# Kernel optimization log

Measured on AMD Instinct MI355X. Metric: run time of the kernel, lower is better.

The kernel has to match this reference:

```python
import jax, jax.numpy as jnp
import numpy as np

N, E, D, H, C = 50000, 800000, 128, 128, 40
EPS = 1e-5


def setup_inputs() -> dict:
    key = jax.random.key(0)
    ks = jax.random.split(key, 18)
    s = lambda d: 1.0 / np.sqrt(d)
    inp = {
        "x": jax.random.normal(ks[0], (N, D), dtype=jnp.float32),
        "edge_index": jax.random.randint(ks[1], (2, E), 0, N, dtype=jnp.int64),
        # GCNConv weights (x @ W + b after normalized aggregation)
        "W1": jax.random.normal(ks[2], (D, H), dtype=jnp.float32) * s(D),
        "b1": jax.random.normal(ks[3], (H,), dtype=jnp.float32) * 0.01,
        "W2": jax.random.normal(ks[4], (H, H), dtype=jnp.float32) * s(H),
        "b2": jax.random.normal(ks[5], (H,), dtype=jnp.float32) * 0.01,
        "W3": jax.random.normal(ks[6], (H, H), dtype=jnp.float32) * s(H),
        "b3": jax.random.normal(ks[7], (H,), dtype=jnp.float32) * 0.01,
        # LayerNorm params (applied after layers 0 and 1 only)
        "ln1_g": 1.0 + 0.1 * jax.random.normal(ks[8], (H,), dtype=jnp.float32),
        "ln1_b": 0.1 * jax.random.normal(ks[9], (H,), dtype=jnp.float32),
        "ln2_g": 1.0 + 0.1 * jax.random.normal(ks[10], (H,), dtype=jnp.float32),
        "ln2_b": 0.1 * jax.random.normal(ks[11], (H,), dtype=jnp.float32),
        # post_mp MLP head
        "mpW1": jax.random.normal(ks[12], (H, H), dtype=jnp.float32) * s(H),
        "mpb1": jax.random.normal(ks[13], (H,), dtype=jnp.float32) * 0.01,
        "mpW2": jax.random.normal(ks[14], (H, C), dtype=jnp.float32) * s(H),
        "mpb2": jax.random.normal(ks[15], (C,), dtype=jnp.float32) * 0.01,
    }
    return inp


def _layernorm(h, g, b):
    mu = jnp.mean(h, axis=-1, keepdims=True)
    var = jnp.mean((h - mu) ** 2, axis=-1, keepdims=True)
    return (h - mu) * jax.lax.rsqrt(var + EPS) * g + b


def _gcn_forward(x, edge_index, params):
    (W1, b1, W2, b2, W3, b3, ln1_g, ln1_b, ln2_g, ln2_b, mpW1, mpb1, mpW2, mpb2) = params
    n = x.shape[0]
    loop = jnp.arange(n, dtype=edge_index.dtype)
    src = jnp.concatenate([edge_index[0], loop])  # source-to-target flow + self-loops
    dst = jnp.concatenate([edge_index[1], loop])
    deg = jax.ops.segment_sum(jnp.ones_like(src, dtype=x.dtype), dst, num_segments=n)
    dis = jax.lax.rsqrt(deg)  # deg >= 1 due to self-loops
    norm = dis[src] * dis[dst]  # [E+N]

    def conv(h, W, b):
        h = h @ W
        msg = h[src] * norm[:, None]  # gather + scale
        return jax.ops.segment_sum(msg, dst, num_segments=n) + b  # scatter-add

    h = x
    # layer 0
    h = conv(h, W1, b1)
    h = jax.nn.relu(h)  # dropout p=0.1 -> identity in eval
    h = _layernorm(h, ln1_g, ln1_b)
    # layer 1
    h = conv(h, W2, b2)
    h = jax.nn.relu(h)
    h = _layernorm(h, ln2_g, ln2_b)
    # layer 2 (emb is pre-relu conv output)
    emb = conv(h, W3, b3)
    h = jax.nn.relu(emb)
    # post_mp: Linear -> Dropout(eval: identity) -> Linear
    h = h @ mpW1 + mpb1
    logits = h @ mpW2 + mpb2
    return emb, jax.nn.log_softmax(logits, axis=1)


def reference(x, edge_index, W1, b1, W2, b2, W3, b3, ln1_g, ln1_b, ln2_g, ln2_b, mpW1, mpb1, mpW2, mpb2):
    params = (W1, b1, W2, b2, W3, b3, ln1_g, ln1_b, ln2_g, ln2_b, mpW1, mpb1, mpW2, mpb2)
    return _gcn_forward(x, edge_index, params)
```

## Files before the change

### kernel.cpp

```cpp
#include <hip/hip_runtime.h>

typedef __bf16 bf16x8 __attribute__((ext_vector_type(8)));
typedef float  f32x4  __attribute__((ext_vector_type(4)));
typedef unsigned short u16;
typedef unsigned int   u32;
typedef long long      i64;

#define BSH  7
#define BCAP 4096
#define NPB  256

__device__ __forceinline__ float b2f(u16 x){ return __uint_as_float(((u32)x) << 16); }
__device__ __forceinline__ u16 f2b(float x){
  u32 u = __float_as_uint(x);
  return (u16)((u + 0x7FFFu + ((u >> 16) & 1u)) >> 16);
}

__global__ __launch_bounds__(256) void k_detect(const u16* __restrict__ x,
                                                const u32* __restrict__ ei,
                                                int* __restrict__ flags){
  __shared__ int sh[2];
  int t = threadIdx.x;
  if (t < 2) sh[t] = 0;
  __syncthreads();
  int sane = 0;
  for (int i = t; i < 4096; i += 256){
    u16 u = x[i]; u32 e = (u >> 7) & 0xFFu;
    if (u == 0 || (e >= 0x70u && e <= 0x8Fu)) sane++;
  }
  int nz = 0;
  for (int i = t; i < 1024; i += 256)
    if (ei[2*i + 1] != 0u) nz++;
  atomicAdd(&sh[0], sane);
  atomicAdd(&sh[1], nz);
  __syncthreads();
  if (t == 0){
    flags[0] = (sh[0] < 3500) ? 1 : 0;
    flags[1] = (sh[1] == 0) ? 1 : 0;
  }
}

__device__ __forceinline__ int ld_idx(const void* ei, long long j, int is64){
  return is64 ? (int)((const i64*)ei)[j] : ((const int*)ei)[j];
}
__device__ __forceinline__ float ld_f(const void* p, int j, int isf32){
  return isf32 ? ((const float*)p)[j] : b2f(((const u16*)p)[j]);
}

__global__ __launch_bounds__(256) void k_partA(const void* __restrict__ ei, int E, int n,
                                               int* __restrict__ cntmat,
                                               const int* __restrict__ flags, int nbuk){
  __shared__ int cnt[512];
  int t = threadIdx.x;
  int is64 = flags[1];
  for (int i = t; i < 512; i += 256) cnt[i] = 0;
  __syncthreads();
  long long R = ((long long)E + NPB - 1) / NPB;
  long long lo = (long long)blockIdx.x * R;
  long long hi = lo + R; if (hi > E) hi = E;
  for (long long e = lo + t; e < hi; e += 256){
    int d = ld_idx(ei, (long long)E + e, is64);
    if ((unsigned)d < (unsigned)n) atomicAdd(&cnt[(unsigned)d >> BSH], 1);
  }
  __syncthreads();
  for (int b = t; b < nbuk; b += 256)
    cntmat[(size_t)b*NPB + blockIdx.x] = cnt[b];
}

__global__ __launch_bounds__(NPB) void k_scanBK(const int* __restrict__ cntmat,
                                                int* __restrict__ basemat,
                                                int* __restrict__ bcnt){
  __shared__ int sh[NPB];
  int b = blockIdx.x, t = threadIdx.x;
  int v = cntmat[(size_t)b*NPB + t];
  sh[t] = v; __syncthreads();
  for (int off = 1; off < NPB; off <<= 1){
    int u = 0; if (t >= off) u = sh[t - off];
    __syncthreads(); sh[t] += u; __syncthreads();
  }
  basemat[(size_t)b*NPB + t] = sh[t] - v;
  if (t == NPB-1) bcnt[b] = sh[t];
}

__global__ __launch_bounds__(256) void k_partC(const void* __restrict__ ei, int E, int n,
                                               const int* __restrict__ basemat,
                                               u32* __restrict__ ebuf,
                                               const int* __restrict__ flags, int nbuk){
  __shared__ int cur[512];
  int t = threadIdx.x;
  int is64 = flags[1];
  for (int i = t; i < 512; i += 256) cur[i] = 0;
  __syncthreads();
  for (int b = t; b < nbuk; b += 256) cur[b] = basemat[(size_t)b*NPB + blockIdx.x];
  __syncthreads();
  long long R = ((long long)E + NPB - 1) / NPB;
  long long lo = (long long)blockIdx.x * R;
  long long hi = lo + R; if (hi > E) hi = E;
  for (long long e = lo + t; e < hi; e += 256){
    int d = ld_idx(ei, (long long)E + e, is64);
    int s = ld_idx(ei, e, is64);
    if ((unsigned)d < (unsigned)n && (unsigned)s < (unsigned)n){
      int b = (unsigned)d >> BSH;
      int p = atomicAdd(&cur[b], 1);
      if (p < BCAP) ebuf[(size_t)b*BCAP + p] = (u32)s | ((u32)(d & ((1<<BSH)-1)) << 17);
    }
  }
}

__global__ __launch_bounds__(256) void k_bdeg(const int* __restrict__ bcnt,
                                              const u32* __restrict__ ebuf,
                                              int* __restrict__ deg, int n){
  __shared__ int cnt[1<<BSH];
  int b = blockIdx.x, t = threadIdx.x;
  if (t < (1<<BSH)) cnt[t] = 0;
  __syncthreads();
  int m = bcnt[b]; if (m > BCAP) m = BCAP;
  const u32* eb = ebuf + (size_t)b*BCAP;
  for (int i = t; i < m; i += 256)
    atomicAdd(&cnt[eb[i] >> 17], 1);
  __syncthreads();
  if (t < (1<<BSH)){
    int node = (b << BSH) + t;
    if (node < n) deg[node] = cnt[t];
  }
}

__global__ __launch_bounds__(256) void k_scanA(const int* __restrict__ deg, int n,
                                               int* __restrict__ bsum){
  __shared__ int sh[256];
  int t = threadIdx.x;
  int base = blockIdx.x*1024 + t*4;
  int s = 0;
  #pragma unroll
  for (int i = 0; i < 4; ++i){ int idx = base + i; if (idx < n) s += deg[idx]; }
  sh[t] = s; __syncthreads();
  for (int off = 128; off; off >>= 1){
    if (t < off) sh[t] += sh[t + off];
    __syncthreads();
  }
  if (t == 0) bsum[blockIdx.x] = sh[0];
}

__global__ __launch_bounds__(256) void k_scanB(int* __restrict__ bsum, int nB,
                                               int* __restrict__ rowptr, int n){
  __shared__ int sh[256];
  int t = threadIdx.x;
  int v = (t < nB) ? bsum[t] : 0;
  sh[t] = v; __syncthreads();
  for (int off = 1; off < 256; off <<= 1){
    int u = 0; if (t >= off) u = sh[t - off];
    __syncthreads(); sh[t] += u; __syncthreads();
  }
  if (t < nB) bsum[t] = sh[t] - v;
  if (t == 255) rowptr[n] = sh[255];
}

__global__ __launch_bounds__(256) void k_scanC(const int* __restrict__ deg, int n,
                                               const int* __restrict__ bsum,
                                               int* __restrict__ rowptr,
                                               float* __restrict__ dis){
  __shared__ int sh[256];
  int t = threadIdx.x;
  int base = blockIdx.x*1024 + t*4;
  int d[4]; int s = 0;
  #pragma unroll
  for (int i = 0; i < 4; ++i){ int idx = base + i; d[i] = (idx < n) ? deg[idx] : 0; s += d[i]; }
  sh[t] = s; __syncthreads();
  for (int off = 1; off < 256; off <<= 1){
    int u = 0; if (t >= off) u = sh[t - off];
    __syncthreads(); sh[t] += u; __syncthreads();
  }
  int run = bsum[blockIdx.x] + sh[t] - s;
  #pragma unroll
  for (int i = 0; i < 4; ++i){
    int idx = base + i;
    if (idx < n){
      rowptr[idx] = run; run += d[i];
      dis[idx] = rsqrtf((float)(d[i] + 1));
    }
  }
}

__global__ __launch_bounds__(256) void k_bfill(const int* __restrict__ bcnt,
                                               const u32* __restrict__ ebuf,
                                               const int* __restrict__ rowptr,
                                               int* __restrict__ colx, int n){
  __shared__ int cur[1<<BSH];
  int b = blockIdx.x, t = threadIdx.x;
  if (t < (1<<BSH)){
    int node = (b << BSH) + t;
    cur[t] = (node < n) ? rowptr[node] : 0;
  }
  __syncthreads();
  int m = bcnt[b]; if (m > BCAP) m = BCAP;
  const u32* eb = ebuf + (size_t)b*BCAP;
  for (int i = t; i < m; i += 256){
    u32 e = eb[i];
    int p = atomicAdd(&cur[e >> 17], 1);
    colx[p] = (int)(e & 0x1FFFFu);
  }
}

__global__ __launch_bounds__(64) void k_shufW(const void* __restrict__ W, u16* __restrict__ Ws,
                                              const int* __restrict__ flags){
  int f = flags[0];
  int bid = blockIdx.x;
  int nt = bid >> 2, kk = bid & 3;
  int l = threadIdx.x;
  int g = l >> 4, mr = l & 15;
  int nn = nt*16 + mr;
  #pragma unroll
  for (int i = 0; i < 8; ++i){
    int k = kk*32 + g*4 + (i & 3) + ((i >> 2) << 4);
    u16 w = f ? f2b(((const float*)W)[k*128 + nn]) : ((const u16*)W)[k*128 + nn];
    Ws[(size_t)(bid*64 + l)*8 + i] = w;
  }
}

__global__ __launch_bounds__(256) void k_gemm(const void* __restrict__ A, int aExt,
    const u16* __restrict__ Ws, const float* __restrict__ dis,
    u16* __restrict__ T, int nTiles, const int* __restrict__ flags)
{
  int wave = threadIdx.x >> 6, lane = threadIdx.x & 63;
  int tile = blockIdx.x*4 + wave;
  if (tile >= nTiles) return;
  int g = lane >> 4, mr = lane & 15;
  int f = aExt ? flags[0] : 0;
  union U8 { ushort4 q[2]; u16 s[8]; bf16x8 b; };
  bf16x8 a[4];
  if (f){
    const float* ap = (const float*)A + (size_t)(tile*16 + mr)*128;
    #pragma unroll
    for (int kk = 0; kk < 4; ++kk){
      float4 p = *(const float4*)(ap + kk*32 + g*4);
      float4 q = *(const float4*)(ap + kk*32 + g*4 + 16);
      U8 u;
      u.s[0]=f2b(p.x); u.s[1]=f2b(p.y); u.s[2]=f2b(p.z); u.s[3]=f2b(p.w);
      u.s[4]=f2b(q.x); u.s[5]=f2b(q.y); u.s[6]=f2b(q.z); u.s[7]=f2b(q.w);
      a[kk] = u.b;
    }
  } else {
    const u16* ap = (const u16*)A + (size_t)(tile*16 + mr)*128;
    #pragma unroll
    for (int kk = 0; kk < 4; ++kk){
      U8 u;
      u.q[0] = *(const ushort4*)(ap + kk*32 + g*4);
      u.q[1] = *(const ushort4*)(ap + kk*32 + g*4 + 16);
      a[kk] = u.b;
    }
  }
  float dj[4];
  #pragma unroll
  for (int j = 0; j < 4; ++j) dj[j] = dis[tile*16 + g*4 + j];
  #pragma unroll
  for (int nt = 0; nt < 8; ++nt){
    f32x4 acc = {0.f,0.f,0.f,0.f};
    #pragma unroll
    for (int kk = 0; kk < 4; ++kk){
      bf16x8 b = *(const bf16x8*)(Ws + (size_t)((nt*4 + kk)*64 + lane)*8);
      acc = __builtin_amdgcn_mfma_f32_16x16x32_bf16(a[kk], b, acc, 0, 0, 0);
    }
    int nn = nt*16 + mr;
    #pragma unroll
    for (int j = 0; j < 4; ++j){
      int row = tile*16 + g*4 + j;
      T[(size_t)row*128 + nn] = f2b(acc[j] * dj[j]);
    }
  }
}

template<int MODE>
__global__ __launch_bounds__(256) void k_agg(const u16* __restrict__ T,
    const int* __restrict__ rowptr, const int* __restrict__ colx,
    const float* __restrict__ dis, const void* __restrict__ bias,
    const void* __restrict__ lg, const void* __restrict__ lb,
    void* __restrict__ outA, int n, const int* __restrict__ flags)
{
  int wave = threadIdx.x >> 6, l = threadIdx.x & 63;
  int v = blockIdx.x*4 + wave; if (v >= n) return;
  int f = flags[0];
  int d0 = l*2;
  u32 self = *(const u32*)(T + (size_t)v*128 + d0);
  float p0 = b2f((u16)(self & 0xffff)), p1 = b2f((u16)(self >> 16));
  float q0 = 0.f, q1 = 0.f, r0 = 0.f, r1 = 0.f, t0 = 0.f, t1 = 0.f;
  int s = rowptr[v], e = rowptr[v+1];
  for (int base = s; base < e; base += 64){
    int cnt = e - base; if (cnt > 64) cnt = 64;
    int my = (base + l < e) ? colx[base + l] : 0;
    int i = 0;
    for (; i + 8 <= cnt; i += 8){
      int nb0 = __shfl(my, i),   nb1 = __shfl(my, i+1);
      int nb2 = __shfl(my, i+2), nb3 = __shfl(my, i+3);
      int nb4 = __shfl(my, i+4), nb5 = __shfl(my, i+5);
      int nb6 = __shfl(my, i+6), nb7 = __shfl(my, i+7);
      u32 u0 = *(const u32*)(T + (size_t)nb0*128 + d0);
      u32 u1 = *(const u32*)(T + (size_t)nb1*128 + d0);
      u32 u2 = *(const u32*)(T + (size_t)nb2*128 + d0);
      u32 u3 = *(const u32*)(T + (size_t)nb3*128 + d0);
      u32 u4 = *(const u32*)(T + (size_t)nb4*128 + d0);
      u32 u5 = *(const u32*)(T + (size_t)nb5*128 + d0);
      u32 u6 = *(const u32*)(T + (size_t)nb6*128 + d0);
      u32 u7 = *(const u32*)(T + (size_t)nb7*128 + d0);
      p0 += b2f((u16)(u0 & 0xffff)) + b2f((u16)(u4 & 0xffff));
      p1 += b2f((u16)(u0 >> 16))    + b2f((u16)(u4 >> 16));
      q0 += b2f((u16)(u1 & 0xffff)) + b2f((u16)(u5 & 0xffff));
      q1 += b2f((u16)(u1 >> 16))    + b2f((u16)(u5 >> 16));
      r0 += b2f((u16)(u2 & 0xffff)) + b2f((u16)(u6 & 0xffff));
      r1 += b2f((u16)(u2 >> 16))    + b2f((u16)(u6 >> 16));
      t0 += b2f((u16)(u3 & 0xffff)) + b2f((u16)(u7 & 0xffff));
      t1 += b2f((u16)(u3 >> 16))    + b2f((u16)(u7 >> 16));
    }
    for (; i + 4 <= cnt; i += 4){
      int nb0 = __shfl(my, i), nb1 = __shfl(my, i+1);
      int nb2 = __shfl(my, i+2), nb3 = __shfl(my, i+3);
      u32 u0 = *(const u32*)(T + (size_t)nb0*128 + d0);
      u32 u1 = *(const u32*)(T + (size_t)nb1*128 + d0);
      u32 u2 = *(const u32*)(T + (size_t)nb2*128 + d0);
      u32 u3 = *(const u32*)(T + (size_t)nb3*128 + d0);
      p0 += b2f((u16)(u0 & 0xffff)); p1 += b2f((u16)(u0 >> 16));
      q0 += b2f((u16)(u1 & 0xffff)); q1 += b2f((u16)(u1 >> 16));
      r0 += b2f((u16)(u2 & 0xffff)); r1 += b2f((u16)(u2 >> 16));
      t0 += b2f((u16)(u3 & 0xffff)); t1 += b2f((u16)(u3 >> 16));
    }
    for (; i < cnt; ++i){
      int nb = __shfl(my, i);
      u32 u = *(const u32*)(T + (size_t)nb*128 + d0);
      p0 += b2f((u16)(u & 0xffff)); p1 += b2f((u16)(u >> 16));
    }
  }
  float a0 = (p0 + q0) + (r0 + t0);
  float a1 = (p1 + q1) + (r1 + t1);
  float sc = dis[v];
  float x0 = fmaf(a0, sc, ld_f(bias, d0,   f));
  float x1 = fmaf(a1, sc, ld_f(bias, d0+1, f));
  if (MODE == 0){
    x0 = fmaxf(x0, 0.f); x1 = fmaxf(x1, 0.f);
    float sum = x0 + x1;
    #pragma unroll
    for (int off = 32; off; off >>= 1) sum += __shfl_xor(sum, off);
    float mu = sum * (1.f/128.f);
    float e0 = x0 - mu, e1 = x1 - mu;
    float vs = e0*e0 + e1*e1;
    #pragma unroll
    for (int off = 32; off; off >>= 1) vs += __shfl_xor(vs, off);
    float inv = rsqrtf(vs*(1.f/128.f) + 1e-5f);
    u16* oa = (u16*)outA;
    oa[(size_t)v*128 + d0]   = f2b(e0*inv*ld_f(lg, d0,   f) + ld_f(lb, d0,   f));
    oa[(size_t)v*128 + d0+1] = f2b(e1*inv*ld_f(lg, d0+1, f) + ld_f(lb, d0+1, f));
  } else {
    if (f){
      float* oa = (float*)outA;
      oa[(size_t)v*128 + d0]   = x0;
      oa[(size_t)v*128 + d0+1] = x1;
    } else {
      u16* oa = (u16*)outA;
      oa[(size_t)v*128 + d0]   = f2b(x0);
      oa[(size_t)v*128 + d0+1] = f2b(x1);
    }
  }
}

__global__ __launch_bounds__(128) void k_wc(const void* __restrict__ mpW1, const void* __restrict__ mpb1,
    const void* __restrict__ mpW2, const void* __restrict__ mpb2,
    float* __restrict__ Wc, float* __restrict__ bc, const int* __restrict__ flags)
{
  int f = flags[0];
  int c = blockIdx.x;
  int k = threadIdx.x;
  float acc = 0.f;
  if (f){
    const float* A  = (const float*)mpW1 + (size_t)k*128;
    const float* B2 = (const float*)mpW2;
    #pragma unroll 8
    for (int j = 0; j < 128; ++j) acc = fmaf(A[j], B2[j*40 + c], acc);
    if (k == 0){
      const float* b1p = (const float*)mpb1;
      float b = ((const float*)mpb2)[c];
      #pragma unroll 8
      for (int j = 0; j < 128; ++j) b = fmaf(b1p[j], B2[j*40 + c], b);
      bc[c] = b;
    }
  } else {
    const u16* A  = (const u16*)mpW1 + (size_t)k*128;
    const u16* B2 = (const u16*)mpW2;
    #pragma unroll 8
    for (int j = 0; j < 128; ++j) acc = fmaf(b2f(A[j]), b2f(B2[j*40 + c]), acc);
    if (k == 0){
      const u16* b1p = (const u16*)mpb1;
      float b = b2f(((const u16*)mpb2)[c]);
      #pragma unroll 8
      for (int j = 0; j < 128; ++j) b = fmaf(b2f(b1p[j]), b2f(B2[j*40 + c]), b);
      bc[c] = b;
    }
  }
  Wc[k*40 + c] = acc;
}

__global__ __launch_bounds__(64) void k_shufWc(const float* __restrict__ Wc, u16* __restrict__ Wcs){
  int bid = blockIdx.x;
  int nt = bid >> 2, kk = bid & 3;
  int l = threadIdx.x;
  int g = l >> 4, mr = l & 15;
  int nn = nt*16 + mr;
  #pragma unroll
  for (int i = 0; i < 8; ++i){
    int k = kk*32 + g*4 + (i & 3) + ((i >> 2) << 4);
    Wcs[(size_t)(bid*64 + l)*8 + i] = (nn < 40) ? f2b(Wc[k*40 + nn]) : (u16)0;
  }
}

__global__ __launch_bounds__(256) void k_logitsM(const u16* __restrict__ Wcs,
    const float* __restrict__ bc, void* __restrict__ dout, int n,
    const int* __restrict__ flags)
{
  int wave = threadIdx.x >> 6, lane = threadIdx.x & 63;
  int tile = blockIdx.x*4 + wave;
  int nTiles = n >> 4;
  if (tile >= nTiles) return;
  int f = flags[0];
  int g = lane >> 4, mr = lane & 15;
  union U8 { ushort4 q[2]; u16 s[8]; bf16x8 b; };
  bf16x8 a[4];
  if (f){
    const float* ap = (const float*)dout + (size_t)(tile*16 + mr)*128;
    #pragma unroll
    for (int kk = 0; kk < 4; ++kk){
      float4 p = *(const float4*)(ap + kk*32 + g*4);
      float4 q = *(const float4*)(ap + kk*32 + g*4 + 16);
      U8 u;
      u.s[0]=f2b(fmaxf(p.x,0.f)); u.s[1]=f2b(fmaxf(p.y,0.f));
      u.s[2]=f2b(fmaxf(p.z,0.f)); u.s[3]=f2b(fmaxf(p.w,0.f));
      u.s[4]=f2b(fmaxf(q.x,0.f)); u.s[5]=f2b(fmaxf(q.y,0.f));
      u.s[6]=f2b(fmaxf(q.z,0.f)); u.s[7]=f2b(fmaxf(q.w,0.f));
      a[kk] = u.b;
    }
  } else {
    const u16* ap = (const u16*)dout + (size_t)(tile*16 + mr)*128;
    #pragma unroll
    for (int kk = 0; kk < 4; ++kk){
      U8 u;
      u.q[0] = *(const ushort4*)(ap + kk*32 + g*4);
      u.q[1] = *(const ushort4*)(ap + kk*32 + g*4 + 16);
      #pragma unroll
      for (int i = 0; i < 8; ++i) u.s[i] = (u.s[i] & 0x8000u) ? (u16)0 : u.s[i];
      a[kk] = u.b;
    }
  }
  f32x4 acc[3];
  #pragma unroll
  for (int nt = 0; nt < 3; ++nt){
    f32x4 c4 = {0.f,0.f,0.f,0.f};
    #pragma unroll
    for (int kk = 0; kk < 4; ++kk){
      bf16x8 b = *(const bf16x8*)(Wcs + (size_t)((nt*4 + kk)*64 + lane)*8);
      c4 = __builtin_amdgcn_mfma_f32_16x16x32_bf16(a[kk], b, c4, 0, 0, 0);
    }
    acc[nt] = c4;
  }
  float bcv[3]; bool valid[3];
  #pragma unroll
  for (int nt = 0; nt < 3; ++nt){
    int c = nt*16 + mr;
    valid[nt] = (c < 40);
    bcv[nt] = valid[nt] ? bc[c] : 0.f;
  }
  float* of = (float*)dout + (size_t)n*128;
  u16*  ob = (u16*) dout + (size_t)n*128;
  #pragma unroll
  for (int j = 0; j < 4; ++j){
    float l0 = valid[0] ? acc[0][j] + bcv[0] : -3.0e38f;
    float l1 = valid[1] ? acc[1][j] + bcv[1] : -3.0e38f;
    float l2 = valid[2] ? acc[2][j] + bcv[2] : -3.0e38f;
    float m = fmaxf(l0, fmaxf(l1, l2));
    #pragma unroll
    for (int off = 8; off; off >>= 1) m = fmaxf(m, __shfl_xor(m, off));
    float ssum = (valid[0] ? expf(l0 - m) : 0.f)
               + (valid[1] ? expf(l1 - m) : 0.f)
               + (valid[2] ? expf(l2 - m) : 0.f);
    #pragma unroll
    for (int off = 8; off; off >>= 1) ssum += __shfl_xor(ssum, off);
    float lgs = m + logf(ssum);
    int node = tile*16 + g*4 + j;
    #pragma unroll
    for (int nt = 0; nt < 3; ++nt){
      if (valid[nt]){
        int c = nt*16 + mr;
        float r = (nt==0 ? l0 : (nt==1 ? l1 : l2)) - lgs;
        if (f) of[(size_t)node*40 + c] = r;
        else   ob[(size_t)node*40 + c] = f2b(r);
      }
    }
  }
}

extern "C" void kernel_launch(void* const* d_in, const int* in_sizes, int n_in,
                              void* d_out, int out_size, void* d_ws, size_t ws_size,
                              hipStream_t stream)
{
  const int n = in_sizes[0] / 128;
  const int E = in_sizes[1] / 2;

  const void* x    = d_in[0];
  const void* ei   = d_in[1];
  const void* W1   = d_in[2];
  const void* b1   = d_in[3];
  const void* W2   = d_in[4];
  const void* b2   = d_in[5];
  const void* W3   = d_in[6];
  const void* b3   = d_in[7];
  const void* ln1g = d_in[8];
  const void* ln1b = d_in[9];
  const void* ln2g = d_in[10];
  const void* ln2b = d_in[11];
  const void* mpW1 = d_in[12];
  const void* mpb1 = d_in[13];
  const void* mpW2 = d_in[14];
  const void* mpb2 = d_in[15];

  u16* Hbuf = (u16*)d_out;

  char* w = (char*)d_ws;
  size_t off = 0;
  auto alloc = [&](size_t bytes)->char*{
    char* p = w + off; off = (off + bytes + 255) & ~(size_t)255; return p;
  };
  const int nbuk = (n + (1<<BSH) - 1) >> BSH;

  int*   flags = (int*)  alloc(256);
  float* dis   = (float*)alloc((size_t)n*4);
  int*   deg   = (int*)  alloc((size_t)n*4);
  int*   rowp  = (int*)  alloc((size_t)(n+1)*4);
  int*   bsum  = (int*)  alloc(1024);
  int*   bcnt  = (int*)  alloc((size_t)nbuk*4);
  int*   cntm  = (int*)  alloc((size_t)nbuk*NPB*4);
  int*   basem = (int*)  alloc((size_t)nbuk*NPB*4);
  u32*   ebuf  = (u32*)  alloc((size_t)nbuk*BCAP*4);
  int*   colx  = (int*)  alloc((size_t)E*4 + 256);
  u16*   T     = (u16*)  alloc((size_t)n*128*2);
  u16*   Ws    = (u16*)  alloc((size_t)128*128*2);
  float* Wc    = (float*)alloc((size_t)128*40*4);
  float* bc    = (float*)alloc((size_t)64*4);
  u16*   Wcs   = (u16*)  alloc((size_t)12*64*8*2);

  int nB = (n + 1023) / 1024;

  k_detect<<<1, 256, 0, stream>>>((const u16*)x, (const u32*)ei, flags);
  k_partA <<<NPB, 256, 0, stream>>>(ei, E, n, cntm, flags, nbuk);
  k_scanBK<<<nbuk, NPB, 0, stream>>>(cntm, basem, bcnt);
  k_partC <<<NPB, 256, 0, stream>>>(ei, E, n, basem, ebuf, flags, nbuk);
  k_bdeg  <<<nbuk, 256, 0, stream>>>(bcnt, ebuf, deg, n);
  k_scanA <<<nB, 256, 0, stream>>>(deg, n, bsum);
  k_scanB <<<1, 256, 0, stream>>>(bsum, nB, rowp, n);
  k_scanC <<<nB, 256, 0, stream>>>(deg, n, bsum, rowp, dis);
  k_bfill <<<nbuk, 256, 0, stream>>>(bcnt, ebuf, rowp, colx, n);
  k_wc    <<<40, 128, 0, stream>>>(mpW1, mpb1, mpW2, mpb2, Wc, bc, flags);
  k_shufWc<<<12, 64, 0, stream>>>(Wc, Wcs);

  int nTiles = (n + 15) / 16;
  int gG = (nTiles + 3) / 4;
  int gA = (n + 3) / 4;

  k_shufW<<<32, 64, 0, stream>>>(W1, Ws, flags);
  k_gemm <<<gG, 256, 0, stream>>>(x, 1, Ws, dis, T, nTiles, flags);
  k_agg<0><<<gA, 256, 0, stream>>>(T, rowp, colx, dis, b1, ln1g, ln1b, Hbuf, n, flags);
  k_shufW<<<32, 64, 0, stream>>>(W2, Ws, flags);
  k_gemm <<<gG, 256, 0, stream>>>(Hbuf, 0, Ws, dis, T, nTiles, flags);
  k_agg<0><<<gA, 256, 0, stream>>>(T, rowp, colx, dis, b2, ln2g, ln2b, Hbuf, n, flags);
  k_shufW<<<32, 64, 0, stream>>>(W3, Ws, flags);
  k_gemm <<<gG, 256, 0, stream>>>(Hbuf, 0, Ws, dis, T, nTiles, flags);
  k_agg<1><<<gA, 256, 0, stream>>>(T, rowp, colx, dis, b3, nullptr, nullptr, d_out, n, flags);
  k_logitsM<<<gG, 256, 0, stream>>>(Wcs, bc, d_out, n, flags);
}
```

Baseline: 237.1 us.

## Store GCN transformed features in fp32 and gather two neighbors per wave with float4

The GEMM now writes the scaled transformed features T in fp32 instead of bf16. The aggregation kernel is reorganised so each half-wave gathers a different neighbor using 16-byte float4 loads, and the halves are combined with a cross-lane shuffle. LayerNorm reductions and output stores are adjusted to the 4-wide-per-lane layout. This cuts per-neighbor instruction count and bf16 unpacking, and improves accuracy, at the cost of doubling the bytes gathered and written for T.

Result: slower. 301.1 us (+27.0%).

```diff
diff --git a/kernel.cpp b/kernel.cpp
--- a/kernel.cpp
+++ b/kernel.cpp
@@ -43,8 +43,15 @@
 __device__ __forceinline__ int ld_idx(const void* ei, long long j, int is64){
   return is64 ? (int)((const i64*)ei)[j] : ((const int*)ei)[j];
 }
-__device__ __forceinline__ float ld_f(const void* p, int j, int isf32){
-  return isf32 ? ((const float*)p)[j] : b2f(((const u16*)p)[j]);
+__device__ __forceinline__ void ld4p(const void* p, int base, int f, float* o){
+  if (f){
+    float4 a = *(const float4*)((const float*)p + base);
+    o[0]=a.x; o[1]=a.y; o[2]=a.z; o[3]=a.w;
+  } else {
+    uint2 q = *(const uint2*)((const u16*)p + base);
+    o[0]=b2f((u16)(q.x&0xffff)); o[1]=b2f((u16)(q.x>>16));
+    o[2]=b2f((u16)(q.y&0xffff)); o[3]=b2f((u16)(q.y>>16));
+  }
 }
 
 __global__ __launch_bounds__(256) void k_partA(const void* __restrict__ ei, int E, int n,
@@ -219,7 +226,7 @@
 
 __global__ __launch_bounds__(256) void k_gemm(const void* __restrict__ A, int aExt,
     const u16* __restrict__ Ws, const float* __restrict__ dis,
-    u16* __restrict__ T, int nTiles, const int* __restrict__ flags)
+    float* __restrict__ T, int nTiles, const int* __restrict__ flags)
 {
   int wave = threadIdx.x >> 6, lane = threadIdx.x & 63;
   int tile = blockIdx.x*4 + wave;
@@ -264,13 +271,13 @@
     #pragma unroll
     for (int j = 0; j < 4; ++j){
       int row = tile*16 + g*4 + j;
-      T[(size_t)row*128 + nn] = f2b(acc[j] * dj[j]);
+      T[(size_t)row*128 + nn] = acc[j] * dj[j];
     }
   }
 }
 
 template<int MODE>
-__global__ __launch_bounds__(256) void k_agg(const u16* __restrict__ T,
+__global__ __launch_bounds__(256) void k_agg(const float* __restrict__ T,
     const int* __restrict__ rowptr, const int* __restrict__ colx,
     const float* __restrict__ dis, const void* __restrict__ bias,
     const void* __restrict__ lg, const void* __restrict__ lb,
@@ -279,83 +286,94 @@
   int wave = threadIdx.x >> 6, l = threadIdx.x & 63;
   int v = blockIdx.x*4 + wave; if (v >= n) return;
   int f = flags[0];
-  int d0 = l*2;
-  u32 self = *(const u32*)(T + (size_t)v*128 + d0);
-  float p0 = b2f((u16)(self & 0xffff)), p1 = b2f((u16)(self >> 16));
-  float q0 = 0.f, q1 = 0.f, r0 = 0.f, r1 = 0.f, t0 = 0.f, t1 = 0.f;
+  int g = l >> 5, c = l & 31;
+  float aA[4], aB[4];
+  if (g == 0){
+    float4 q = *(const float4*)(T + (size_t)v*128 + c*4);
+    aA[0]=q.x; aA[1]=q.y; aA[2]=q.z; aA[3]=q.w;
+  } else {
+    aA[0]=0.f; aA[1]=0.f; aA[2]=0.f; aA[3]=0.f;
+  }
+  aB[0]=0.f; aB[1]=0.f; aB[2]=0.f; aB[3]=0.f;
+
   int s = rowptr[v], e = rowptr[v+1];
   for (int base = s; base < e; base += 64){
     int cnt = e - base; if (cnt > 64) cnt = 64;
     int my = (base + l < e) ? colx[base + l] : 0;
     int i = 0;
     for (; i + 8 <= cnt; i += 8){
-      int nb0 = __shfl(my, i),   nb1 = __shfl(my, i+1);
-      int nb2 = __shfl(my, i+2), nb3 = __shfl(my, i+3);
-      int nb4 = __shfl(my, i+4), nb5 = __shfl(my, i+5);
-      int nb6 = __shfl(my, i+6), nb7 = __shfl(my, i+7);
-      u32 u0 = *(const u32*)(T + (size_t)nb0*128 + d0);
-      u32 u1 = *(const u32*)(T + (size_t)nb1*128 + d0);
-      u32 u2 = *(const u32*)(T + (size_t)nb2*128 + d0);
-      u32 u3 = *(const u32*)(T + (size_t)nb3*128 + d0);
-      u32 u4 = *(const u32*)(T + (size_t)nb4*128 + d0);
-      u32 u5 = *(const u32*)(T + (size_t)nb5*128 + d0);
-      u32 u6 = *(const u32*)(T + (size_t)nb6*128 + d0);
-      u32 u7 = *(const u32*)(T + (size_t)nb7*128 + d0);
-      p0 += b2f((u16)(u0 & 0xffff)) + b2f((u16)(u4 & 0xffff));
-      p1 += b2f((u16)(u0 >> 16))    + b2f((u16)(u4 >> 16));
-      q0 += b2f((u16)(u1 & 0xffff)) + b2f((u16)(u5 & 0xffff));
-      q1 += b2f((u16)(u1 >> 16))    + b2f((u16)(u5 >> 16));
-      r0 += b2f((u16)(u2 & 0xffff)) + b2f((u16)(u6 & 0xffff));
-      r1 += b2f((u16)(u2 >> 16))    + b2f((u16)(u6 >> 16));
-      t0 += b2f((u16)(u3 & 0xffff)) + b2f((u16)(u7 & 0xffff));
-      t1 += b2f((u16)(u3 >> 16))    + b2f((u16)(u7 >> 16));
-    }
-    for (; i + 4 <= cnt; i += 4){
-      int nb0 = __shfl(my, i), nb1 = __shfl(my, i+1);
-      int nb2 = __shfl(my, i+2), nb3 = __shfl(my, i+3);
-      u32 u0 = *(const u32*)(T + (size_t)nb0*128 + d0);
-      u32 u1 = *(const u32*)(T + (size_t)nb1*128 + d0);
-      u32 u2 = *(const u32*)(T + (size_t)nb2*128 + d0);
-      u32 u3 = *(const u32*)(T + (size_t)nb3*128 + d0);
-      p0 += b2f((u16)(u0 & 0xffff)); p1 += b2f((u16)(u0 >> 16));
-      q0 += b2f((u16)(u1 & 0xffff)); q1 += b2f((u16)(u1 >> 16));
-      r0 += b2f((u16)(u2 & 0xffff)); r1 += b2f((u16)(u2 >> 16));
-      t0 += b2f((u16)(u3 & 0xffff)); t1 += b2f((u16)(u3 >> 16));
-    }
-    for (; i < cnt; ++i){
+      int nb0 = __shfl(my, i + g);
+      int nb1 = __shfl(my, i + 2 + g);
+      int nb2 = __shfl(my, i + 4 + g);
+      int nb3 = __shfl(my, i + 6 + g);
+      float4 q0 = *(const float4*)(T + (size_t)nb0*128 + c*4);
+      float4 q1 = *(const float4*)(T + (size_t)nb1*128 + c*4);
+      float4 q2 = *(const float4*)(T + (size_t)nb2*128 + c*4);
+      float4 q3 = *(const float4*)(T + (size_t)nb3*128 + c*4);
+      aA[0]+=q0.x; aA[1]+=q0.y; aA[2]+=q0.z; aA[3]+=q0.w;
+      aB[0]+=q1.x; aB[1]+=q1.y; aB[2]+=q1.z; aB[3]+=q1.w;
+      aA[0]+=q2.x; aA[1]+=q2.y; aA[2]+=q2.z; aA[3]+=q2.w;
+      aB[0]+=q3.x; aB[1]+=q3.y; aB[2]+=q3.z; aB[3]+=q3.w;
+    }
+    for (; i + 2 <= cnt; i += 2){
+      int nb = __shfl(my, i + g);
+      float4 q = *(const float4*)(T + (size_t)nb*128 + c*4);
+      aA[0]+=q.x; aA[1]+=q.y; aA[2]+=q.z; aA[3]+=q.w;
+    }
+    if (i < cnt){
       int nb = __shfl(my, i);
-      u32 u = *(const u32*)(T + (size_t)nb*128 + d0);
-      p0 += b2f((u16)(u & 0xffff)); p1 += b2f((u16)(u >> 16));
-    }
-  }
-  float a0 = (p0 + q0) + (r0 + t0);
-  float a1 = (p1 + q1) + (r1 + t1);
+      if (g == 0){
+        float4 q = *(const float4*)(T + (size_t)nb*128 + c*4);
+        aA[0]+=q.x; aA[1]+=q.y; aA[2]+=q.z; aA[3]+=q.w;
+      }
+    }
+  }
+  float acc[4];
+  #pragma unroll
+  for (int k = 0; k < 4; ++k){
+    float t2 = aA[k] + aB[k];
+    t2 += __shfl_xor(t2, 32);
+    acc[k] = t2;
+  }
   float sc = dis[v];
-  float x0 = fmaf(a0, sc, ld_f(bias, d0,   f));
-  float x1 = fmaf(a1, sc, ld_f(bias, d0+1, f));
+  float bv[4]; ld4p(bias, c*4, f, bv);
+  float x[4];
+  #pragma unroll
+  for (int k = 0; k < 4; ++k) x[k] = fmaf(acc[k], sc, bv[k]);
+
   if (MODE == 0){
-    x0 = fmaxf(x0, 0.f); x1 = fmaxf(x1, 0.f);
-    float sum = x0 + x1;
-    #pragma unroll
-    for (int off = 32; off; off >>= 1) sum += __shfl_xor(sum, off);
+    #pragma unroll
+    for (int k = 0; k < 4; ++k) x[k] = fmaxf(x[k], 0.f);
+    float sum = (x[0] + x[1]) + (x[2] + x[3]);
+    #pragma unroll
+    for (int off = 16; off; off >>= 1) sum += __shfl_xor(sum, off);
     float mu = sum * (1.f/128.f);
-    float e0 = x0 - mu, e1 = x1 - mu;
-    float vs = e0*e0 + e1*e1;
-    #pragma unroll
-    for (int off = 32; off; off >>= 1) vs += __shfl_xor(vs, off);
+    float vs = 0.f;
+    #pragma unroll
+    for (int k = 0; k < 4; ++k){ float d = x[k] - mu; vs += d*d; }
+    #pragma unroll
+    for (int off = 16; off; off >>= 1) vs += __shfl_xor(vs, off);
     float inv = rsqrtf(vs*(1.f/128.f) + 1e-5f);
-    u16* oa = (u16*)outA;
-    oa[(size_t)v*128 + d0]   = f2b(e0*inv*ld_f(lg, d0,   f) + ld_f(lb, d0,   f));
-    oa[(size_t)v*128 + d0+1] = f2b(e1*inv*ld_f(lg, d0+1, f) + ld_f(lb, d0+1, f));
+    float gv[4], bvv[4];
+    ld4p(lg, c*4, f, gv); ld4p(lb, c*4, f, bvv);
+    if (g == 0){
+      uint2 w;
+      float y0 = (x[0]-mu)*inv*gv[0] + bvv[0], y1 = (x[1]-mu)*inv*gv[1] + bvv[1];
+      w.x = (u32)f2b(y0) | ((u32)f2b(y1) << 16);
+      float y2 = (x[2]-mu)*inv*gv[2] + bvv[2], y3 = (x[3]-mu)*inv*gv[3] + bvv[3];
+      w.y = (u32)f2b(y2) | ((u32)f2b(y3) << 16);
+      *(uint2*)((u16*)outA + (size_t)v*128 + c*4) = w;
+    }
   } else {
-    if (f){
-      float* oa = (float*)outA;
-      oa[(size_t)v*128 + d0]   = x0;
-      oa[(size_t)v*128 + d0+1] = x1;
-    } else {
-      u16* oa = (u16*)outA;
-      oa[(size_t)v*128 + d0]   = f2b(x0);
-      oa[(size_t)v*128 + d0+1] = f2b(x1);
+    if (g == 0){
+      if (f){
+        *(float4*)((float*)outA + (size_t)v*128 + c*4) = make_float4(x[0], x[1], x[2], x[3]);
+      } else {
+        uint2 w;
+        w.x = (u32)f2b(x[0]) | ((u32)f2b(x[1]) << 16);
+        w.y = (u32)f2b(x[2]) | ((u32)f2b(x[3]) << 16);
+        *(uint2*)((u16*)outA + (size_t)v*128 + c*4) = w;
+      }
     }
   }
 }
@@ -536,7 +554,7 @@
   int*   basem = (int*)  alloc((size_t)nbuk*NPB*4);
   u32*   ebuf  = (u32*)  alloc((size_t)nbuk*BCAP*4);
   int*   colx  = (int*)  alloc((size_t)E*4 + 256);
-  u16*   T     = (u16*)  alloc((size_t)n*128*2);
+  float* T     = (float*)alloc((size_t)n*128*4);
   u16*   Ws    = (u16*)  alloc((size_t)128*128*2);
   float* Wc    = (float*)alloc((size_t)128*40*4);
   float* bc    = (float*)alloc((size_t)64*4);
```
